# Kernel tuning notes

Hardware: AMD Instinct MI355X
Metric: run time of the kernel (lower is better)

## Reference

```python
import jax, jax.numpy as jnp
import numpy as np
import math

DIM = 512
HEADS = 8
K_SEEDS = 4
HEAD_DIM = DIM // HEADS
EPS = 1e-6


def setup_inputs() -> dict:
    key = jax.random.key(0)
    ks = jax.random.split(key, 12)
    B, N = 16, 8192
    s = 1.0 / math.sqrt(DIM)
    inp = {
        "X": jax.random.normal(ks[0], (B, N, DIM), dtype=jnp.float32),
        "seed": jax.random.normal(ks[1], (1, K_SEEDS, DIM), dtype=jnp.float32),
        "Wq": jax.random.uniform(ks[2], (DIM, DIM), minval=-s, maxval=s),
        "bq": jax.random.uniform(ks[3], (DIM,), minval=-s, maxval=s),
        "Wk": jax.random.uniform(ks[4], (DIM, DIM), minval=-s, maxval=s),
        "bk": jax.random.uniform(ks[5], (DIM,), minval=-s, maxval=s),
        "Wv": jax.random.uniform(ks[6], (DIM, DIM), minval=-s, maxval=s),
        "bv": jax.random.uniform(ks[7], (DIM,), minval=-s, maxval=s),
        "Wo": jax.random.uniform(ks[8], (DIM, DIM), minval=-s, maxval=s),
        "bo": jax.random.uniform(ks[9], (DIM,), minval=-s, maxval=s),
        "gamma": jnp.ones((DIM,), dtype=jnp.float32),
        "beta": jnp.zeros((DIM,), dtype=jnp.float32),
    }
    return inp


def reference(X, seed, Wq, bq, Wk, bk, Wv, bv, Wo, bo, gamma, beta):
    B, N, _ = X.shape
    S = jnp.broadcast_to(seed, (B, K_SEEDS, DIM))  # expanded seed vectors
    # QKV projections (torch Linear: x @ W.T + b)
    q = (S @ Wq.T + bq).reshape(B, K_SEEDS, HEADS, HEAD_DIM)
    k = (X @ Wk.T + bk).reshape(B, N, HEADS, HEAD_DIM)
    v = (X @ Wv.T + bv).reshape(B, N, HEADS, HEAD_DIM)
    # scores: [B, H, Kq, N]
    scores = jnp.einsum("bqhd,bnhd->bhqn", q, k) / math.sqrt(HEAD_DIM)
    attn = jax.nn.softmax(scores, axis=-1)
    out = jnp.einsum("bhqn,bnhd->bqhd", attn, v).reshape(B, K_SEEDS, DIM)
    out = out @ Wo.T + bo
    # residual + LayerNorm
    h = out + S
    mu = jnp.mean(h, axis=-1, keepdims=True)
    var = jnp.mean((h - mu) ** 2, axis=-1, keepdims=True)
    return (h - mu) * jax.lax.rsqrt(var + EPS) * gamma + beta
```

## Files before the change

### kernel.cpp

```cpp
#include <hip/hip_runtime.h>
#include <math.h>

#define DIM 512
#define KQn 4
#define HQ  32
#define BB  16
#define NN  8192
#define EPSLN 1e-6f
#define TROWS  32

typedef _Float16 f16;
typedef _Float16 h2_t __attribute__((ext_vector_type(2)));
typedef __fp16   g2_t __attribute__((ext_vector_type(2)));
typedef _Float16 h8_t __attribute__((ext_vector_type(8)));
typedef float    f32x4 __attribute__((ext_vector_type(4)));

union U32H2 { unsigned int u; h2_t h; g2_t g; };
union U4H8  { uint4 u; h8_t h; unsigned int w[4]; };

__device__ inline unsigned int pkh2(float a, float b) {
    U32H2 v; v.g = __builtin_amdgcn_cvt_pkrtz(a, b); return v.u;
}
__device__ inline h2_t ash2(unsigned int u) { U32H2 v; v.u = u; return v.h; }

__global__ __launch_bounds__(256) void k_q(
    const float* __restrict__ seed, const float* __restrict__ Wq,
    const float* __restrict__ bq, float* __restrict__ q_g)
{
    int hq = blockIdx.x; int h = hq >> 2; int j = hq & 3;
    int t = threadIdx.x;
    __shared__ float qpart[256];
    int d = t >> 2, q4 = t & 3;
    const float* sr = seed + j*DIM + q4*128;
    const float* wr = Wq + (size_t)(h*64 + d)*DIM + q4*128;
    float acc = 0.f;
    for (int c = 0; c < 128; c += 4) {
        float4 s4 = *(const float4*)(sr + c);
        float4 w4 = *(const float4*)(wr + c);
        acc += s4.x*w4.x + s4.y*w4.y + s4.z*w4.z + s4.w*w4.w;
    }
    qpart[t] = acc;
    __syncthreads();
    if (t < 64)
        q_g[hq*64 + t] = qpart[t*4] + qpart[t*4+1] + qpart[t*4+2] + qpart[t*4+3] + bq[h*64 + t];
}

__global__ __launch_bounds__(256) void k_qk(
    const float* __restrict__ Wk, const float* __restrict__ q_g, f16* __restrict__ qkB)
{
    const int h = blockIdx.x;
    const int cs = blockIdx.y;
    const int t = threadIdx.x;
    __shared__ float q_s[4][64];
    __shared__ float red2[4][128];
    q_s[t >> 6][t & 63] = q_g[(h*4 + (t >> 6))*64 + (t & 63)];
    __syncthreads();
    const int c = cs*128 + (t & 127);
    const int dh = t >> 7;
    float a0=0.f, a1=0.f, a2=0.f, a3=0.f;
    const float* wb = Wk + ((size_t)(h*64 + dh*32))*DIM + c;
    #pragma unroll 8
    for (int d = 0; d < 32; ++d) {
        float w = wb[(size_t)d*DIM];
        a0 += q_s[0][dh*32 + d]*w;
        a1 += q_s[1][dh*32 + d]*w;
        a2 += q_s[2][dh*32 + d]*w;
        a3 += q_s[3][dh*32 + d]*w;
    }
    if (dh == 1) {
        red2[0][t & 127] = a0; red2[1][t & 127] = a1;
        red2[2][t & 127] = a2; red2[3][t & 127] = a3;
    }
    __syncthreads();
    if (dh == 0) {
        int ci = t & 127;
        float v[4];
        v[0] = (a0 + red2[0][ci]) * 0.125f;
        v[1] = (a1 + red2[1][ci]) * 0.125f;
        v[2] = (a2 + red2[2][ci]) * 0.125f;
        v[3] = (a3 + red2[3][ci]) * 0.125f;
        const int kb = c >> 5, g = (c >> 3) & 3, ii = c & 7;
        #pragma unroll
        for (int j = 0; j < 4; ++j) {
            const int hq = h*4 + j;
            const int nb = hq >> 4, lane = g*16 + (hq & 15);
            qkB[(((size_t)(kb*2 + nb)*64 + lane) << 3) + ii] = (f16)v[j];
        }
    }
}

__global__ __launch_bounds__(256, 4) void k_att(
    const float* __restrict__ X, const f16* __restrict__ qkB,
    f16* __restrict__ opart, float* __restrict__ lpart,
    int nchunk, int crows, int ntile)
{
    const int chunk = blockIdx.x, b = blockIdx.y;
    const int t = threadIdx.x;

    __shared__ f16 Xcm[512][36];
    __shared__ f16 p_s[32][40];
    __shared__ float lred[256];

    unsigned int* XcmU = (unsigned int*)&Xcm[0][0];
    unsigned int* pW   = (unsigned int*)&p_s[0][0];

    const int w    = t >> 6;
    const int lane = t & 63;
    const int mb = w & 1, nb = w >> 1;
    const int lg = lane >> 4;
    const int lm = lane & 15;

    const int rp = t >> 4;
    const int cq = (t & 15) << 1;

    f32x4 o_acc[8][2];
    #pragma unroll
    for (int cb = 0; cb < 8; ++cb) {
        #pragma unroll
        for (int hb = 0; hb < 2; ++hb)
            o_acc[cb][hb] = (f32x4){0.f,0.f,0.f,0.f};
    }
    float l_local = 0.f;

    const size_t xbase = (size_t)b*NN*DIM;
    const uint4* qkB4 = (const uint4*)qkB;

    for (int tile = 0; tile < ntile; ++tile) {
        const int r0 = chunk*crows + tile*TROWS;
        __syncthreads();
        {
            const float2* Xr0 = (const float2*)(X + xbase + (size_t)(r0 + rp*2    )*DIM);
            const float2* Xr1 = (const float2*)(X + xbase + (size_t)(r0 + rp*2 + 1)*DIM);
            #pragma unroll
            for (int cs = 0; cs < 16; ++cs) {
                int c0 = cs*32 + cq;
                float2 xa = Xr0[c0 >> 1];
                float2 xb = Xr1[c0 >> 1];
                XcmU[c0*18 + rp]     = pkh2(xa.x, xb.x);
                XcmU[(c0+1)*18 + rp] = pkh2(xa.y, xb.y);
            }
        }
        {
            const float* xr = X + xbase + (size_t)(r0 + mb*16 + lm)*DIM + lg*8;
            f32x4 acc0 = {0.f,0.f,0.f,0.f}, acc1 = {0.f,0.f,0.f,0.f};
            #pragma unroll
            for (int kb = 0; kb < 16; ++kb) {
                float4 a0 = *(const float4*)(xr + kb*32);
                float4 a1 = *(const float4*)(xr + kb*32 + 4);
                U4H8 af;
                af.w[0] = pkh2(a0.x, a0.y); af.w[1] = pkh2(a0.z, a0.w);
                af.w[2] = pkh2(a1.x, a1.y); af.w[3] = pkh2(a1.z, a1.w);
                U4H8 bf; bf.u = qkB4[(size_t)(kb*2 + nb)*64 + lane];
                if (kb & 1) acc1 = __builtin_amdgcn_mfma_f32_16x16x32_f16(af.h, bf.h, acc1, 0, 0, 0);
                else        acc0 = __builtin_amdgcn_mfma_f32_16x16x32_f16(af.h, bf.h, acc0, 0, 0, 0);
            }
            float p0 = __expf(fminf(acc0[0] + acc1[0], 30.f));
            float p1 = __expf(fminf(acc0[1] + acc1[1], 30.f));
            float p2 = __expf(fminf(acc0[2] + acc1[2], 30.f));
            float p3 = __expf(fminf(acc0[3] + acc1[3], 30.f));
            l_local += p0 + p1 + p2 + p3;
            const int pidx = (nb*16 + lm)*20 + mb*8 + lg*2;
            pW[pidx]     = pkh2(p0, p1);
            pW[pidx + 1] = pkh2(p2, p3);
        }
        __syncthreads();
        {
            U4H8 bf0, bf1;
            const int pbase = lm*20 + lg*4;
            bf0.u = *(const uint4*)&pW[pbase];
            bf1.u = *(const uint4*)&pW[320 + pbase];
            #pragma unroll
            for (int cb = 0; cb < 8; ++cb) {
                const int c = (w*8 + cb)*16 + lm;
                const unsigned int* row = &XcmU[c*18 + lg*4];
                uint2 xa = *(const uint2*)&row[0];
                uint2 xb = *(const uint2*)&row[2];
                U4H8 af;
                af.w[0] = xa.x; af.w[1] = xa.y; af.w[2] = xb.x; af.w[3] = xb.y;
                o_acc[cb][0] = __builtin_amdgcn_mfma_f32_16x16x32_f16(af.h, bf0.h, o_acc[cb][0], 0, 0, 0);
                o_acc[cb][1] = __builtin_amdgcn_mfma_f32_16x16x32_f16(af.h, bf1.h, o_acc[cb][1], 0, 0, 0);
            }
        }
    }
    __syncthreads();
    lred[t] = l_local;
    unsigned int* otU = (unsigned int*)&Xcm[0][0];
    #pragma unroll
    for (int cb = 0; cb < 8; ++cb) {
        const int chalf = ((w*8 + cb)*16 + lg*4) >> 1;
        #pragma unroll
        for (int hb = 0; hb < 2; ++hb) {
            const int hq = hb*16 + lm;
            otU[hq*260 + chalf]     = pkh2(o_acc[cb][hb][0], o_acc[cb][hb][1]);
            otU[hq*260 + chalf + 1] = pkh2(o_acc[cb][hb][2], o_acc[cb][hb][3]);
        }
    }
    __syncthreads();
    if (t < 32) {
        const int nb2 = t >> 4, col = t & 15;
        float l = 0.f;
        #pragma unroll
        for (int mm = 0; mm < 2; ++mm)
            #pragma unroll
            for (int g = 0; g < 4; ++g)
                l += lred[(nb2*2 + mm)*64 + g*16 + col];
        lpart[((size_t)b*nchunk + chunk)*HQ + t] = l;
    }
    {
        const int hq_w = t >> 3, c0 = (t & 7) << 6;
        const unsigned int* src = &otU[hq_w*260 + (c0 >> 1)];
        f16* dst = opart + (((size_t)b*nchunk + chunk)*HQ + hq_w)*DIM + c0;
        #pragma unroll
        for (int i = 0; i < 4; ++i)
            *(uint4*)(dst + i*16) = *(const uint4*)(src + i*8);
    }
}

__global__ __launch_bounds__(256) void k_red(
    const f16* __restrict__ opart, const float* __restrict__ lpart,
    const float* __restrict__ Wv, const float* __restrict__ bv,
    float* __restrict__ vbuf, int nchunk)
{
    const int hq = blockIdx.x, b = blockIdx.y;
    const int h = hq >> 2, j = hq & 3;
    const int t = threadIdx.x;
    __shared__ float pool_s[512];
    __shared__ float linv_s;
    if (t < 64) {
        float l = (t < nchunk) ? lpart[((size_t)b*nchunk + t)*HQ + hq] : 0.f;
        #pragma unroll
        for (int m = 1; m < 64; m <<= 1) l += __shfl_xor(l, m);
        if (t == 0) linv_s = 1.f / l;
    }
    float a0 = 0.f, a1 = 0.f;
    const unsigned int* opU = (const unsigned int*)opart;
    #pragma unroll 4
    for (int ch = 0; ch < nchunk; ++ch) {
        unsigned int u = opU[((((size_t)b*nchunk + ch)*HQ + hq) << 8) + t];
        h2_t hv = ash2(u);
        a0 += (float)hv.x; a1 += (float)hv.y;
    }
    __syncthreads();
    float linv = linv_s;
    pool_s[2*t]   = a0 * linv;
    pool_s[2*t+1] = a1 * linv;
    __syncthreads();
    const int o1 = t >> 2, q4 = t & 3;
    const float* wr = Wv + ((size_t)(h*64 + o1))*DIM + q4*128;
    const float* ps = pool_s + q4*128;
    float acc = 0.f;
    #pragma unroll 8
    for (int c = 0; c < 128; c += 4) {
        float4 w4 = *(const float4*)(wr + c);
        float4 p4 = *(const float4*)(ps + c);
        acc += w4.x*p4.x + w4.y*p4.y + w4.z*p4.z + w4.w*p4.w;
    }
    acc += __shfl_xor(acc, 1);
    acc += __shfl_xor(acc, 2);
    if (q4 == 0)
        vbuf[((size_t)b*KQn + j)*DIM + h*64 + o1] = acc + bv[h*64 + o1];
}

__global__ __launch_bounds__(512) void k_wo_ln(
    const float* __restrict__ vbuf, const float* __restrict__ Wo, const float* __restrict__ bo,
    const float* __restrict__ seed, const float* __restrict__ gamma, const float* __restrict__ beta,
    float* __restrict__ out)
{
    const int j = blockIdx.x, b = blockIdx.y;
    const int t = threadIdx.x;
    __shared__ float v_s[512];
    __shared__ float wsum[8], wsq[8];
    v_s[t] = vbuf[((size_t)b*KQn + j)*DIM + t];
    __syncthreads();
    const float* wr = Wo + (size_t)t*DIM;
    float acc = bo[t];
    #pragma unroll 8
    for (int c = 0; c < 512; c += 4) {
        float4 w4 = *(const float4*)(wr + c);
        float4 p4 = *(const float4*)&v_s[c];
        acc += w4.x*p4.x + w4.y*p4.y + w4.z*p4.z + w4.w*p4.w;
    }
    float hv = acc + seed[j*DIM + t];
    float s1 = hv, s2 = hv*hv;
    #pragma unroll
    for (int m = 1; m <= 32; m <<= 1) {
        s1 += __shfl_xor(s1, m);
        s2 += __shfl_xor(s2, m);
    }
    if ((t & 63) == 0) { wsum[t >> 6] = s1; wsq[t >> 6] = s2; }
    __syncthreads();
    float tm = 0.f, tq = 0.f;
    #pragma unroll
    for (int i = 0; i < 8; ++i) { tm += wsum[i]; tq += wsq[i]; }
    float mu = tm * (1.f/512.f);
    float var = tq * (1.f/512.f) - mu*mu;
    float rs = rsqrtf(var + EPSLN);
    out[((size_t)b*KQn + j)*DIM + t] = (hv - mu)*rs*gamma[t] + beta[t];
}

extern "C" void kernel_launch(void* const* d_in, const int* in_sizes, int n_in,
                              void* d_out, int out_size, void* d_ws, size_t ws_size,
                              hipStream_t stream) {
    const float* X     = (const float*)d_in[0];
    const float* seed  = (const float*)d_in[1];
    const float* Wq    = (const float*)d_in[2];
    const float* bq    = (const float*)d_in[3];
    const float* Wk    = (const float*)d_in[4];
    const float* Wv    = (const float*)d_in[6];
    const float* bv    = (const float*)d_in[7];
    const float* Wo    = (const float*)d_in[8];
    const float* bo    = (const float*)d_in[9];
    const float* gamma = (const float*)d_in[10];
    const float* beta  = (const float*)d_in[11];

    int nchunk = 64;
    {
        const size_t need64 = 303104UL + (size_t)BB*64*HQ*DIM*2;
        if (ws_size < need64) nchunk = 32;
    }
    const int crows = NN / nchunk;
    const int ntile = crows / TROWS;

    char* ws = (char*)d_ws;
    float* q_g   = (float*)(ws + 0);
    f16*   qkB   = (f16*)  (ws + 8192);
    size_t off_lpart = 40960;
    size_t off_vbuf  = off_lpart + (size_t)BB*nchunk*HQ*4;
    size_t off_opart = off_vbuf + (size_t)BB*KQn*DIM*4;
    float* lpart = (float*)(ws + off_lpart);
    float* vbuf  = (float*)(ws + off_vbuf);
    f16*   opart = (f16*)  (ws + off_opart);
    float* out   = (float*)d_out;

    k_q    <<<32,               256, 0, stream>>>(seed, Wq, bq, q_g);
    k_qk   <<<dim3(8, 4),       256, 0, stream>>>(Wk, q_g, qkB);
    k_att  <<<dim3(nchunk, BB), 256, 0, stream>>>(X, qkB, opart, lpart, nchunk, crows, ntile);
    k_red  <<<dim3(HQ, BB),     256, 0, stream>>>(opart, lpart, Wv, bv, vbuf, nchunk);
    k_wo_ln<<<dim3(KQn, BB),    512, 0, stream>>>(vbuf, Wo, bo, seed, gamma, beta, out);
}
```

Measured before the change: 536.5 us.

## Double-buffer X tiles into LDS via async global_load_lds in attention kernel

The attention kernel now stages 16-row fp32 X tiles into swizzled, double-buffered LDS with async global-to-LDS loads, prefetching the next tile while the current one is consumed. The QK product is split across wave pairs with a shared-memory reduction, and query-key fragments are hoisted into registers once per block. This removes the second global read of X and the separate transpose-to-fp16 staging. In exchange it uses more LDS, lowers the occupancy target to 2 blocks per CU, pads the P tile with zeros, and fixes the partial-output copy so it covers every column.

```diff
diff --git a/kernel.cpp b/kernel.cpp
--- a/kernel.cpp
+++ b/kernel.cpp
@@ -7,7 +7,7 @@
 #define BB  16
 #define NN  8192
 #define EPSLN 1e-6f
-#define TROWS  32
+#define STROWS 16
 
 typedef _Float16 f16;
 typedef _Float16 h2_t __attribute__((ext_vector_type(2)));
@@ -22,6 +22,13 @@
     U32H2 v; v.g = __builtin_amdgcn_cvt_pkrtz(a, b); return v.u;
 }
 __device__ inline h2_t ash2(unsigned int u) { U32H2 v; v.u = u; return v.h; }
+
+typedef __attribute__((address_space(3))) unsigned char lds_uc;
+typedef __attribute__((address_space(1))) const unsigned char gbl_uc;
+
+__device__ inline void gload_lds16(const float* g, void* l) {
+    __builtin_amdgcn_global_load_lds((gbl_uc*)g, (lds_uc*)l, 16, 0, 0);
+}
 
 __global__ __launch_bounds__(256) void k_q(
     const float* __restrict__ seed, const float* __restrict__ Wq,
@@ -89,7 +96,7 @@
     }
 }
 
-__global__ __launch_bounds__(256, 4) void k_att(
+__global__ __launch_bounds__(256, 2) void k_att(
     const float* __restrict__ X, const f16* __restrict__ qkB,
     f16* __restrict__ opart, float* __restrict__ lpart,
     int nchunk, int crows, int ntile)
@@ -97,94 +104,117 @@
     const int chunk = blockIdx.x, b = blockIdx.y;
     const int t = threadIdx.x;
 
-    __shared__ f16 Xcm[512][36];
-    __shared__ f16 p_s[32][40];
+    __shared__ __align__(16) float Xbuf[2][STROWS*512];
+    __shared__ __align__(16) f16 p_s[32][40];
+    __shared__ __align__(16) float sred[2][64][4];
     __shared__ float lred[256];
 
-    unsigned int* XcmU = (unsigned int*)&Xcm[0][0];
-    unsigned int* pW   = (unsigned int*)&p_s[0][0];
-
-    const int w    = t >> 6;
-    const int lane = t & 63;
-    const int mb = w & 1, nb = w >> 1;
-    const int lg = lane >> 4;
-    const int lm = lane & 15;
-
-    const int rp = t >> 4;
-    const int cq = (t & 15) << 1;
+    unsigned int* pW = (unsigned int*)&p_s[0][0];
+
+    const int w = t >> 6, lane = t & 63;
+    const int nb = w & 1, kh = w >> 1;
+    const int lg = lane >> 4, lm = lane & 15;
 
     f32x4 o_acc[8][2];
     #pragma unroll
     for (int cb = 0; cb < 8; ++cb) {
-        #pragma unroll
-        for (int hb = 0; hb < 2; ++hb)
-            o_acc[cb][hb] = (f32x4){0.f,0.f,0.f,0.f};
+        o_acc[cb][0] = (f32x4){0.f,0.f,0.f,0.f};
+        o_acc[cb][1] = (f32x4){0.f,0.f,0.f,0.f};
     }
     float l_local = 0.f;
 
     const size_t xbase = (size_t)b*NN*DIM;
+
+    uint4 bfA[8];
     const uint4* qkB4 = (const uint4*)qkB;
+    #pragma unroll
+    for (int j = 0; j < 8; ++j)
+        bfA[j] = qkB4[(size_t)((kh*8 + j)*2 + nb)*64 + lane];
+
+    pW[(t >> 3)*20 + 8 + (t & 7)] = 0u;
+
+    #define STAGE(bufi, tile_)                                                          \
+    {                                                                                   \
+        const int r0s = chunk*crows + (tile_)*STROWS;                                   \
+        _Pragma("unroll")                                                               \
+        for (int j = 0; j < 8; ++j) {                                                   \
+            const int i = w*8 + j;                                                      \
+            const int row = i >> 1, half = i & 1;                                       \
+            const float* gp = X + xbase + (size_t)(r0s + row)*DIM                       \
+                              + ((half*64 + (lane ^ (row & 7))) << 2);                  \
+            void* lp = (void*)((char*)&Xbuf[bufi][0] + i*1024);                         \
+            gload_lds16(gp, lp);                                                        \
+        }                                                                               \
+    }
+
+    STAGE(0, 0)
+    __syncthreads();
+    int cur = 0;
 
     for (int tile = 0; tile < ntile; ++tile) {
-        const int r0 = chunk*crows + tile*TROWS;
+        const float* xb = &Xbuf[cur][0];
+        f32x4 part;
+        {
+            f32x4 acc0 = {0.f,0.f,0.f,0.f}, acc1 = {0.f,0.f,0.f,0.f};
+            const int swzA = lm & 7;
+            const float* rowp = xb + lm*512;
+            #pragma unroll
+            for (int j = 0; j < 8; ++j) {
+                const int kb = kh*8 + j;
+                const int pg0 = (kb*8 + lg*2) ^ swzA;
+                f32x4 xv0 = *(const f32x4*)(rowp + (pg0 << 2));
+                f32x4 xv1 = *(const f32x4*)(rowp + ((pg0 ^ 1) << 2));
+                U4H8 af;
+                af.w[0] = pkh2(xv0[0], xv0[1]); af.w[1] = pkh2(xv0[2], xv0[3]);
+                af.w[2] = pkh2(xv1[0], xv1[1]); af.w[3] = pkh2(xv1[2], xv1[3]);
+                U4H8 bf; bf.u = bfA[j];
+                if (j & 1) acc1 = __builtin_amdgcn_mfma_f32_16x16x32_f16(af.h, bf.h, acc1, 0, 0, 0);
+                else       acc0 = __builtin_amdgcn_mfma_f32_16x16x32_f16(af.h, bf.h, acc0, 0, 0, 0);
+            }
+            part = acc0 + acc1;
+        }
+        if (kh == 1) *(f32x4*)&sred[nb][lane][0] = part;
         __syncthreads();
-        {
-            const float2* Xr0 = (const float2*)(X + xbase + (size_t)(r0 + rp*2    )*DIM);
-            const float2* Xr1 = (const float2*)(X + xbase + (size_t)(r0 + rp*2 + 1)*DIM);
-            #pragma unroll
-            for (int cs = 0; cs < 16; ++cs) {
-                int c0 = cs*32 + cq;
-                float2 xa = Xr0[c0 >> 1];
-                float2 xb = Xr1[c0 >> 1];
-                XcmU[c0*18 + rp]     = pkh2(xa.x, xb.x);
-                XcmU[(c0+1)*18 + rp] = pkh2(xa.y, xb.y);
-            }
-        }
-        {
-            const float* xr = X + xbase + (size_t)(r0 + mb*16 + lm)*DIM + lg*8;
-            f32x4 acc0 = {0.f,0.f,0.f,0.f}, acc1 = {0.f,0.f,0.f,0.f};
-            #pragma unroll
-            for (int kb = 0; kb < 16; ++kb) {
-                float4 a0 = *(const float4*)(xr + kb*32);
-                float4 a1 = *(const float4*)(xr + kb*32 + 4);
-                U4H8 af;
-                af.w[0] = pkh2(a0.x, a0.y); af.w[1] = pkh2(a0.z, a0.w);
-                af.w[2] = pkh2(a1.x, a1.y); af.w[3] = pkh2(a1.z, a1.w);
-                U4H8 bf; bf.u = qkB4[(size_t)(kb*2 + nb)*64 + lane];
-                if (kb & 1) acc1 = __builtin_amdgcn_mfma_f32_16x16x32_f16(af.h, bf.h, acc1, 0, 0, 0);
-                else        acc0 = __builtin_amdgcn_mfma_f32_16x16x32_f16(af.h, bf.h, acc0, 0, 0, 0);
-            }
-            float p0 = __expf(fminf(acc0[0] + acc1[0], 30.f));
-            float p1 = __expf(fminf(acc0[1] + acc1[1], 30.f));
-            float p2 = __expf(fminf(acc0[2] + acc1[2], 30.f));
-            float p3 = __expf(fminf(acc0[3] + acc1[3], 30.f));
+        if (kh == 0) {
+            f32x4 o = *(const f32x4*)&sred[nb][lane][0];
+            float p0 = __expf(fminf(part[0] + o[0], 30.f));
+            float p1 = __expf(fminf(part[1] + o[1], 30.f));
+            float p2 = __expf(fminf(part[2] + o[2], 30.f));
+            float p3 = __expf(fminf(part[3] + o[3], 30.f));
             l_local += p0 + p1 + p2 + p3;
-            const int pidx = (nb*16 + lm)*20 + mb*8 + lg*2;
+            const int pidx = (nb*16 + lm)*20 + lg*2;
             pW[pidx]     = pkh2(p0, p1);
             pW[pidx + 1] = pkh2(p2, p3);
         }
         __syncthreads();
+        if (tile + 1 < ntile) STAGE(cur ^ 1, tile + 1)
         {
             U4H8 bf0, bf1;
-            const int pbase = lm*20 + lg*4;
-            bf0.u = *(const uint4*)&pW[pbase];
-            bf1.u = *(const uint4*)&pW[320 + pbase];
+            bf0.u = *(const uint4*)&pW[lm*20 + lg*4];
+            bf1.u = *(const uint4*)&pW[(16 + lm)*20 + lg*4];
             #pragma unroll
             for (int cb = 0; cb < 8; ++cb) {
                 const int c = (w*8 + cb)*16 + lm;
-                const unsigned int* row = &XcmU[c*18 + lg*4];
-                uint2 xa = *(const uint2*)&row[0];
-                uint2 xb = *(const uint2*)&row[2];
+                const int cg = c >> 2, cr = c & 3;
+                float xv[8];
+                #pragma unroll
+                for (int i = 0; i < 8; ++i) {
+                    const int nn = (8*lg + i) & 15;
+                    xv[i] = xb[nn*512 + (((cg ^ (nn & 7)) << 2) | cr)];
+                }
                 U4H8 af;
-                af.w[0] = xa.x; af.w[1] = xa.y; af.w[2] = xb.x; af.w[3] = xb.y;
+                af.w[0] = pkh2(xv[0], xv[1]); af.w[1] = pkh2(xv[2], xv[3]);
+                af.w[2] = pkh2(xv[4], xv[5]); af.w[3] = pkh2(xv[6], xv[7]);
                 o_acc[cb][0] = __builtin_amdgcn_mfma_f32_16x16x32_f16(af.h, bf0.h, o_acc[cb][0], 0, 0, 0);
                 o_acc[cb][1] = __builtin_amdgcn_mfma_f32_16x16x32_f16(af.h, bf1.h, o_acc[cb][1], 0, 0, 0);
             }
         }
-    }
-    __syncthreads();
+        __syncthreads();
+        cur ^= 1;
+    }
+
     lred[t] = l_local;
-    unsigned int* otU = (unsigned int*)&Xcm[0][0];
+    unsigned int* otU = (unsigned int*)&Xbuf[0][0];
     #pragma unroll
     for (int cb = 0; cb < 8; ++cb) {
         const int chalf = ((w*8 + cb)*16 + lg*4) >> 1;
@@ -197,13 +227,10 @@
     }
     __syncthreads();
     if (t < 32) {
-        const int nb2 = t >> 4, col = t & 15;
         float l = 0.f;
         #pragma unroll
-        for (int mm = 0; mm < 2; ++mm)
-            #pragma unroll
-            for (int g = 0; g < 4; ++g)
-                l += lred[(nb2*2 + mm)*64 + g*16 + col];
+        for (int g = 0; g < 4; ++g)
+            l += lred[(t >> 4)*64 + g*16 + (t & 15)];
         lpart[((size_t)b*nchunk + chunk)*HQ + t] = l;
     }
     {
@@ -211,9 +238,10 @@
         const unsigned int* src = &otU[hq_w*260 + (c0 >> 1)];
         f16* dst = opart + (((size_t)b*nchunk + chunk)*HQ + hq_w)*DIM + c0;
         #pragma unroll
-        for (int i = 0; i < 4; ++i)
-            *(uint4*)(dst + i*16) = *(const uint4*)(src + i*8);
-    }
+        for (int i = 0; i < 8; ++i)
+            *(uint4*)(dst + i*8) = *(const uint4*)(src + i*4);
+    }
+    #undef STAGE
 }
 
 __global__ __launch_bounds__(256) void k_red(
@@ -319,7 +347,7 @@
         if (ws_size < need64) nchunk = 32;
     }
     const int crows = NN / nchunk;
-    const int ntile = crows / TROWS;
+    const int ntile = crows / STROWS;
 
     char* ws = (char*)d_ws;
     float* q_g   = (float*)(ws + 0);
```

Result: faster. 448.9 us (-16.3%).
